# Kernel optimization log

Measured on AMD Instinct MI355X. Metric: run time of the kernel, lower is better.

## Reference

```python
import jax, jax.numpy as jnp
import numpy as np

COMMITMENT_COST = 0.25


def setup_inputs() -> dict:
    key = jax.random.key(0)
    k1, k2 = jax.random.split(key)
    z_e = jax.random.normal(k1, (32, 256, 32, 32), dtype=jnp.float32)
    codebook = jax.random.normal(k2, (1024, 256), dtype=jnp.float32)
    return {"z_e": z_e, "codebook": codebook}


def reference(z_e, codebook):
    B, D, H, W = z_e.shape
    # (B, D, H, W) -> (N, D), N = B*H*W
    z_flat = jnp.transpose(z_e, (0, 2, 3, 1)).reshape(-1, D)
    # squared L2 distances to every codebook entry: (N, K)
    distances = (
        jnp.sum(z_flat * z_flat, axis=1, keepdims=True)
        - 2.0 * (z_flat @ codebook.T)
        + jnp.sum(codebook * codebook, axis=1)
    )
    codes = jnp.argmin(distances, axis=1)          # (N,)
    z_q = jnp.transpose(codebook[codes].reshape(B, H, W, D), (0, 3, 1, 2))
    # straight-through estimator
    z_q_st = z_e + jax.lax.stop_gradient(z_q - z_e)
    codebook_loss = jnp.mean((jax.lax.stop_gradient(z_q) - z_e) ** 2)
    commitment_loss = jnp.mean((z_q - jax.lax.stop_gradient(z_e)) ** 2)
    vq_loss = codebook_loss + COMMITMENT_COST * commitment_loss
    indices = codes.reshape(B, H, W)
    return z_q_st, indices, vq_loss
```

## Files before the change

### kernel.cpp

```cpp
#include <hip/hip_runtime.h>
#include <cstdint>
#include <cstddef>


typedef __attribute__((ext_vector_type(8))) short bf16x8;
typedef __attribute__((ext_vector_type(4))) float f32x4;

#define GL2LDS(g, l) __builtin_amdgcn_global_load_lds( \
    (__attribute__((address_space(1))) const void*)(g), \
    (__attribute__((address_space(3))) void*)(l), 16, 0, 0)

__device__ __forceinline__ unsigned short rne_bf16(float f) {
    unsigned u = __float_as_uint(f);
    return (unsigned short)((u + 0x7FFFu + ((u >> 16) & 1u)) >> 16);
}
__device__ __forceinline__ float bf16_to_f(unsigned short h) {
    return __uint_as_float((unsigned)h << 16);
}

__global__ __launch_bounds__(256)
void vq_cnorm_kernel(const float* __restrict__ cb, float* __restrict__ cnorm)
{
    const int k = blockIdx.x * 256 + threadIdx.x;
    const float4* row = reinterpret_cast<const float4*>(cb + (size_t)k * 256);
    float s0 = 0.f, s1 = 0.f, s2 = 0.f, s3 = 0.f;
#pragma unroll 8
    for (int i = 0; i < 64; ++i) {
        float4 v = row[i];
        s0 = fmaf(v.x, v.x, s0);
        s1 = fmaf(v.y, v.y, s1);
        s2 = fmaf(v.z, v.z, s2);
        s3 = fmaf(v.w, v.w, s3);
    }
    cnorm[k] = (s0 + s1) + (s2 + s3);
}

__global__ __launch_bounds__(256)
void vq_csplit_kernel(const float* __restrict__ cb, unsigned short* __restrict__ c0,
                      unsigned short* __restrict__ c1, unsigned short* __restrict__ c2,
                      unsigned long long* __restrict__ packed, float* __restrict__ loss)
{
    const int b = blockIdx.x, t = threadIdx.x;
    const int idx = b * 256 + t;
    if (t < 128) packed[b * 128 + t] = 0xFFFFFFFFFFFFFFFFull;
    if (b == 0 && t == 255) *loss = 0.f;

    float4 v = reinterpret_cast<const float4*>(cb)[idx];
    float f[4] = { v.x, v.y, v.z, v.w };
    ushort4 h0, h1, h2;
    unsigned short* p0[4] = { &h0.x, &h0.y, &h0.z, &h0.w };
    unsigned short* p1[4] = { &h1.x, &h1.y, &h1.z, &h1.w };
    unsigned short* p2[4] = { &h2.x, &h2.y, &h2.z, &h2.w };
#pragma unroll
    for (int j = 0; j < 4; ++j) {
        unsigned short b0 = rne_bf16(f[j]); float r1 = f[j] - bf16_to_f(b0);
        unsigned short b1 = rne_bf16(r1);   float r2 = r1 - bf16_to_f(b1);
        unsigned short b2 = rne_bf16(r2);
        *p0[j] = b0; *p1[j] = b1; *p2[j] = b2;
    }
    reinterpret_cast<ushort4*>(c0)[idx] = h0;
    reinterpret_cast<ushort4*>(c1)[idx] = h1;
    reinterpret_cast<ushort4*>(c2)[idx] = h2;
}

__global__ __launch_bounds__(256)
void vq_zsplit_kernel(const float* __restrict__ z, unsigned short* __restrict__ z0,
                      unsigned short* __restrict__ z1, unsigned short* __restrict__ z2)
{
    __shared__ float zl[64 * 264];
    const int t = threadIdx.x, blk = blockIdx.x;
    const int b = blk >> 4, hw0 = (blk & 15) << 6;
    const float* zb = z + ((size_t)b << 18) + hw0;
#pragma unroll 8
    for (int i = 0; i < 64; ++i) {
        int idx = i * 256 + t;
        int d = idx >> 6, hwl = idx & 63;
        zl[hwl * 264 + d] = zb[(size_t)d * 1024 + hwl];
    }
    __syncthreads();
    const int n0 = (b << 10) + hw0;
#pragma unroll
    for (int p = 0; p < 8; ++p) {
        const int hwl = p * 8 + (t >> 5);
        const int d0 = (t & 31) * 8;
        const float* src = &zl[hwl * 264 + d0];
        unsigned short h0[8], h1[8], h2[8];
#pragma unroll
        for (int j = 0; j < 8; ++j) {
            float f = src[j];
            unsigned short b0 = rne_bf16(f);  float r1 = f - bf16_to_f(b0);
            unsigned short b1 = rne_bf16(r1); float r2 = r1 - bf16_to_f(b1);
            unsigned short b2 = rne_bf16(r2);
            h0[j] = b0; h1[j] = b1; h2[j] = b2;
        }
        const size_t o = (size_t)(n0 + hwl) * 256 + d0;
        ushort4 a;
        a = ushort4{h0[0],h0[1],h0[2],h0[3]}; *reinterpret_cast<ushort4*>(z0 + o)     = a;
        a = ushort4{h0[4],h0[5],h0[6],h0[7]}; *reinterpret_cast<ushort4*>(z0 + o + 4) = a;
        a = ushort4{h1[0],h1[1],h1[2],h1[3]}; *reinterpret_cast<ushort4*>(z1 + o)     = a;
        a = ushort4{h1[4],h1[5],h1[6],h1[7]}; *reinterpret_cast<ushort4*>(z1 + o + 4) = a;
        a = ushort4{h2[0],h2[1],h2[2],h2[3]}; *reinterpret_cast<ushort4*>(z2 + o)     = a;
        a = ushort4{h2[4],h2[5],h2[6],h2[7]}; *reinterpret_cast<ushort4*>(z2 + o + 4) = a;
    }
}

__global__ __launch_bounds__(512, 1)
void vq_mfma_argmin_kernel(const unsigned short* __restrict__ zp,
                           const unsigned short* __restrict__ cp,
                           const float* __restrict__ cnorm,
                           unsigned long long* __restrict__ packed)
{
    __shared__ unsigned short Ld[3 * 24576];

    const int tid = threadIdx.x, l = tid & 63, w = tid >> 6;
    const int wr = w >> 1, wc = w & 1;
    const int nid = ((blockIdx.x & 7) << 7) | (blockIdx.x >> 3);
    const int bm = nid >> 3, bn = nid & 7;
    const int arow = bm * 256, brow = bn * 128;

    f32x4 acc[4][4];
#pragma unroll
    for (int m = 0; m < 4; ++m)
#pragma unroll
        for (int n = 0; n < 4; ++n) acc[m][n] = f32x4{0.f, 0.f, 0.f, 0.f};

    const int srow  = l >> 2;
    const int selem = (((l & 3) ^ ((l >> 3) & 3))) << 3;

    const int lo16 = l & 15, hi4 = l >> 4;
    const int fco = ((hi4 ^ ((lo16 >> 1) & 3))) << 3;

#define STAGE6(tt, BUFP) do {                                                 \
    const int seg_ = (tt) >> 2;                                               \
    const unsigned short* As_ = zp + (size_t)((0x010210 >> (seg_ << 2)) & 3) * 8388608u; \
    const unsigned short* Bs_ = cp + (size_t)((0x211000 >> (seg_ << 2)) & 3) * 262144u;  \
    const int KO_ = (((tt) & 3) << 6) + selem;                                \
    GL2LDS(As_ + (size_t)(arow + w * 32 +  0 + srow) * 256 + KO_,      (BUFP) + (w * 32     ) * 32); \
    GL2LDS(As_ + (size_t)(arow + w * 32 + 16 + srow) * 256 + KO_,      (BUFP) + (w * 32 + 16) * 32); \
    GL2LDS(As_ + (size_t)(arow + w * 32 +  0 + srow) * 256 + KO_ + 32, (BUFP) + 8192 + (w * 32     ) * 32); \
    GL2LDS(As_ + (size_t)(arow + w * 32 + 16 + srow) * 256 + KO_ + 32, (BUFP) + 8192 + (w * 32 + 16) * 32); \
    GL2LDS(Bs_ + (size_t)(brow + w * 16 + srow) * 256 + KO_,           (BUFP) + 16384 + (w * 16) * 32); \
    GL2LDS(Bs_ + (size_t)(brow + w * 16 + srow) * 256 + KO_ + 32,      (BUFP) + 16384 + 4096 + (w * 16) * 32); \
} while (0)

#define VM6  asm volatile("s_waitcnt vmcnt(6)"  ::: "memory")
#define VM0  asm volatile("s_waitcnt vmcnt(0)"  ::: "memory")
#define NOPS ((void)0)
#define FNCE do { asm volatile("" ::: "memory");                              \
                  __builtin_amdgcn_sched_barrier(0); } while (0)
#define SBAR do { asm volatile("" ::: "memory");                              \
                  __builtin_amdgcn_s_barrier();                               \
                  __builtin_amdgcn_sched_barrier(0); } while (0)

#define MFMA16(A0, A1, A2, A3, B0, B1, B2, B3)                                \
    acc[0][0] = __builtin_amdgcn_mfma_f32_16x16x32_bf16(A0, B0, acc[0][0], 0,0,0); \
    acc[0][1] = __builtin_amdgcn_mfma_f32_16x16x32_bf16(A0, B1, acc[0][1], 0,0,0); \
    acc[0][2] = __builtin_amdgcn_mfma_f32_16x16x32_bf16(A0, B2, acc[0][2], 0,0,0); \
    acc[0][3] = __builtin_amdgcn_mfma_f32_16x16x32_bf16(A0, B3, acc[0][3], 0,0,0); \
    acc[1][0] = __builtin_amdgcn_mfma_f32_16x16x32_bf16(A1, B0, acc[1][0], 0,0,0); \
    acc[1][1] = __builtin_amdgcn_mfma_f32_16x16x32_bf16(A1, B1, acc[1][1], 0,0,0); \
    acc[1][2] = __builtin_amdgcn_mfma_f32_16x16x32_bf16(A1, B2, acc[1][2], 0,0,0); \
    acc[1][3] = __builtin_amdgcn_mfma_f32_16x16x32_bf16(A1, B3, acc[1][3], 0,0,0); \
    acc[2][0] = __builtin_amdgcn_mfma_f32_16x16x32_bf16(A2, B0, acc[2][0], 0,0,0); \
    acc[2][1] = __builtin_amdgcn_mfma_f32_16x16x32_bf16(A2, B1, acc[2][1], 0,0,0); \
    acc[2][2] = __builtin_amdgcn_mfma_f32_16x16x32_bf16(A2, B2, acc[2][2], 0,0,0); \
    acc[2][3] = __builtin_amdgcn_mfma_f32_16x16x32_bf16(A2, B3, acc[2][3], 0,0,0); \
    acc[3][0] = __builtin_amdgcn_mfma_f32_16x16x32_bf16(A3, B0, acc[3][0], 0,0,0); \
    acc[3][1] = __builtin_amdgcn_mfma_f32_16x16x32_bf16(A3, B1, acc[3][1], 0,0,0); \
    acc[3][2] = __builtin_amdgcn_mfma_f32_16x16x32_bf16(A3, B2, acc[3][2], 0,0,0); \
    acc[3][3] = __builtin_amdgcn_mfma_f32_16x16x32_bf16(A3, B3, acc[3][3], 0,0,0)

#define PH_T(BUFP, STAGESTMT, VMSTMT, BARSTMT) do {                           \
    const unsigned short* Ap_ = (BUFP);                                       \
    const unsigned short* Bp_ = (BUFP) + 16384;                               \
    bf16x8 a0, a1, a2, a3, b0, b1, b2, b3;                                    \
    a0 = *(const bf16x8*)&Ap_[(wr*64 + 0*16 + lo16)*32 + fco];                \
    a1 = *(const bf16x8*)&Ap_[(wr*64 + 1*16 + lo16)*32 + fco];                \
    a2 = *(const bf16x8*)&Ap_[(wr*64 + 2*16 + lo16)*32 + fco];                \
    a3 = *(const bf16x8*)&Ap_[(wr*64 + 3*16 + lo16)*32 + fco];                \
    b0 = *(const bf16x8*)&Bp_[(wc*64 + 0*16 + lo16)*32 + fco];                \
    b1 = *(const bf16x8*)&Bp_[(wc*64 + 1*16 + lo16)*32 + fco];                \
    b2 = *(const bf16x8*)&Bp_[(wc*64 + 2*16 + lo16)*32 + fco];                \
    b3 = *(const bf16x8*)&Bp_[(wc*64 + 3*16 + lo16)*32 + fco];                \
    STAGESTMT;                                                                \
    FNCE;                                                                     \
    __builtin_amdgcn_s_setprio(1);                                            \
    MFMA16(a0, a1, a2, a3, b0, b1, b2, b3);                                   \
    __builtin_amdgcn_s_setprio(0);                                            \
    a0 = *(const bf16x8*)&Ap_[8192 + (wr*64 + 0*16 + lo16)*32 + fco];         \
    a1 = *(const bf16x8*)&Ap_[8192 + (wr*64 + 1*16 + lo16)*32 + fco];         \
    a2 = *(const bf16x8*)&Ap_[8192 + (wr*64 + 2*16 + lo16)*32 + fco];         \
    a3 = *(const bf16x8*)&Ap_[8192 + (wr*64 + 3*16 + lo16)*32 + fco];         \
    b0 = *(const bf16x8*)&Bp_[4096 + (wc*64 + 0*16 + lo16)*32 + fco];         \
    b1 = *(const bf16x8*)&Bp_[4096 + (wc*64 + 1*16 + lo16)*32 + fco];         \
    b2 = *(const bf16x8*)&Bp_[4096 + (wc*64 + 2*16 + lo16)*32 + fco];         \
    b3 = *(const bf16x8*)&Bp_[4096 + (wc*64 + 3*16 + lo16)*32 + fco];         \
    FNCE;                                                                     \
    __builtin_amdgcn_s_setprio(1);                                            \
    MFMA16(a0, a1, a2, a3, b0, b1, b2, b3);                                   \
    __builtin_amdgcn_s_setprio(0);                                            \
    VMSTMT;                                                                   \
    BARSTMT;                                                                  \
} while (0)

    STAGE6(0, Ld);
    STAGE6(1, Ld + 24576);
    VM6;
    SBAR;

    for (int t = 0; t < 21; t += 3) {
        PH_T(Ld,             STAGE6(t + 2, Ld + 2 * 24576), VM6, SBAR);
        PH_T(Ld + 24576,     STAGE6(t + 3, Ld),             VM6, SBAR);
        PH_T(Ld + 2 * 24576, STAGE6(t + 4, Ld + 24576),     VM6, SBAR);
    }
    PH_T(Ld,             STAGE6(23, Ld + 2 * 24576), VM6, SBAR);
    PH_T(Ld + 24576,     NOPS,                       VM0, SBAR);
    PH_T(Ld + 2 * 24576, NOPS,                       NOPS, NOPS);

#undef PH_T
#undef MFMA16
#undef STAGE6

    int coln[4]; float cnv[4];
#pragma unroll
    for (int n = 0; n < 4; ++n) {
        coln[n] = brow + wc * 64 + n * 16 + lo16;
        cnv[n] = cnorm[coln[n]];
    }
#pragma unroll
    for (int m = 0; m < 4; ++m) {
#pragma unroll
        for (int j = 0; j < 4; ++j) {
            unsigned long long best = 0xFFFFFFFFFFFFFFFFull;
#pragma unroll
            for (int n = 0; n < 4; ++n) {
                float d = fmaf(-2.0f, acc[m][n][j], cnv[n]);
                unsigned u = __float_as_uint(d);
                u = (u & 0x80000000u) ? ~u : (u | 0x80000000u);
                unsigned long long pk = ((unsigned long long)u << 32) | (unsigned)coln[n];
                best = pk < best ? pk : best;
            }
#pragma unroll
            for (int mask = 1; mask <= 8; mask <<= 1) {
                unsigned long long o = __shfl_xor(best, mask, 64);
                best = o < best ? o : best;
            }
            if (lo16 == 0) {
                const int row = arow + wr * 64 + m * 16 + hi4 * 4 + j;
                atomicMin(&packed[row], best);
            }
        }
    }
}

__global__ __launch_bounds__(256, 2)
void vq_gather_packed_kernel(const float* __restrict__ cb, const float* __restrict__ z,
                             const unsigned long long* __restrict__ packed,
                             float* __restrict__ out_zq, float* __restrict__ out_idx,
                             float* __restrict__ loss)
{
    __shared__ float rows[64 * 257];
    __shared__ int   ks[64];
    __shared__ float wsum[4];

    const int t   = threadIdx.x;
    const int blk = blockIdx.x;
    const int b   = blk >> 4;
    const int hw0 = (blk & 15) << 6;
    const int n0  = blk << 6;

    if (t < 64) {
        const int k = (int)(packed[n0 + t] & 0xFFFFFFFFull);
        ks[t] = k;
        out_idx[n0 + t] = (float)k;
    }
    __syncthreads();

#pragma unroll 4
    for (int i = 0; i < 64; ++i) {
        rows[i * 257 + t] = cb[(size_t)ks[i] * 256 + t];
    }
    __syncthreads();

    const int dq = t >> 6;
    const int hw = t & 63;
    const size_t obase = ((size_t)b << 18) + hw0 + hw;
    float sum = 0.f;
#pragma unroll 4
    for (int dd = 0; dd < 64; ++dd) {
        const int d = (dq << 6) + dd;
        const float  q  = rows[hw * 257 + d];
        const size_t a  = obase + (size_t)d * 1024;
        const float  zv = z[a];
        out_zq[a] = q;
        const float diff = q - zv;
        sum = fmaf(diff, diff, sum);
    }
#pragma unroll
    for (int m = 1; m <= 32; m <<= 1) sum += __shfl_xor(sum, m, 64);
    if ((t & 63) == 0) wsum[t >> 6] = sum;
    __syncthreads();
    if (t == 0) {
        const float s = (wsum[0] + wsum[1]) + (wsum[2] + wsum[3]);
        atomicAdd(loss, s * (1.25f / 8388608.0f));
    }
}

__global__ __launch_bounds__(256)
void vq_transpose_kernel(const float* __restrict__ cb, float* __restrict__ ctT)
{
    __shared__ float tile[64 * 65];
    const int t  = threadIdx.x;
    const int kb = blockIdx.x >> 2, db = blockIdx.x & 3;
    const int k0 = kb << 6, d0 = db << 6;
#pragma unroll
    for (int i = 0; i < 16; ++i) {
        int idx = i * 256 + t;
        int r = idx >> 6, c = idx & 63;
        tile[r * 65 + c] = cb[(size_t)(k0 + r) * 256 + d0 + c];
    }
    __syncthreads();
#pragma unroll
    for (int i = 0; i < 16; ++i) {
        int idx = i * 256 + t;
        int r = idx >> 6, c = idx & 63;
        ctT[(size_t)(d0 + r) * 1024 + k0 + c] = tile[c * 65 + r];
    }
}

__global__ __launch_bounds__(256)
void vq_cnorm_fb_kernel(const float* __restrict__ cb, float* __restrict__ cnorm)
{
    const int k = blockIdx.x * 256 + threadIdx.x;
    const float4* row = reinterpret_cast<const float4*>(cb + (size_t)k * 256);
    float s0 = 0.f, s1 = 0.f, s2 = 0.f, s3 = 0.f;
#pragma unroll 8
    for (int i = 0; i < 64; ++i) {
        float4 v = row[i];
        s0 = fmaf(v.x, v.x, s0);
        s1 = fmaf(v.y, v.y, s1);
        s2 = fmaf(v.z, v.z, s2);
        s3 = fmaf(v.w, v.w, s3);
    }
    cnorm[k] = (s0 + s1) + (s2 + s3);
}

__global__ __launch_bounds__(512, 2)
void vq_argmin_kernel(const float* __restrict__ z, const float* __restrict__ ctT,
                      const float* __restrict__ cnorm, int* __restrict__ codes,
                      float* __restrict__ out_idx)
{
    __shared__ float zt[256 * 64];
    __shared__ float ct[16 * 256];
    const int t = threadIdx.x, tx = t & 63, ty = t >> 6, p0 = ty << 3;
    const int blk = blockIdx.x, b = blk >> 4, hw0 = (blk & 15) << 6;
    const float* zbase = z + ((size_t)b << 18) + hw0;
#pragma unroll
    for (int i = 0; i < 8; ++i) {
        int idx = i * 512 + t;
        int d = idx >> 4, c4 = (idx & 15) << 2;
        float4 v = *reinterpret_cast<const float4*>(zbase + (size_t)d * 1024 + c4);
        *reinterpret_cast<float4*>(&zt[d * 64 + c4]) = v;
    }
    float minv[8]; int mini[8];
#pragma unroll
    for (int i = 0; i < 8; ++i) { minv[i] = 3.0e38f; mini[i] = 0; }
    const float* zrd = &zt[p0];
    const float* crd = &ct[tx << 2];
    for (int kt = 0; kt < 4; ++kt) {
        const int k0 = kt << 8;
        float acc[8][4];
#pragma unroll
        for (int i = 0; i < 8; ++i)
#pragma unroll
            for (int j = 0; j < 4; ++j) acc[i][j] = 0.f;
        for (int dc = 0; dc < 16; ++dc) {
            const int d0 = dc << 4;
            __syncthreads();
#pragma unroll
            for (int i = 0; i < 2; ++i) {
                int idx = i * 512 + t;
                int r = idx >> 6, c4 = (idx & 63) << 2;
                float4 v = *reinterpret_cast<const float4*>(ctT + (size_t)(d0 + r) * 1024 + k0 + c4);
                *reinterpret_cast<float4*>(&ct[r * 256 + c4]) = v;
            }
            __syncthreads();
            const float* zp = zrd + d0 * 64;
#pragma unroll
            for (int d = 0; d < 16; ++d) {
                float4 za = *reinterpret_cast<const float4*>(zp + d * 64);
                float4 zb = *reinterpret_cast<const float4*>(zp + d * 64 + 4);
                float4 cc = *reinterpret_cast<const float4*>(crd + d * 256);
#define VQ_FMA_ROW(ii, zv)                          \
                acc[ii][0] = fmaf(zv, cc.x, acc[ii][0]); \
                acc[ii][1] = fmaf(zv, cc.y, acc[ii][1]); \
                acc[ii][2] = fmaf(zv, cc.z, acc[ii][2]); \
                acc[ii][3] = fmaf(zv, cc.w, acc[ii][3]);
                VQ_FMA_ROW(0, za.x) VQ_FMA_ROW(1, za.y) VQ_FMA_ROW(2, za.z) VQ_FMA_ROW(3, za.w)
                VQ_FMA_ROW(4, zb.x) VQ_FMA_ROW(5, zb.y) VQ_FMA_ROW(6, zb.z) VQ_FMA_ROW(7, zb.w)
#undef VQ_FMA_ROW
            }
        }
#pragma unroll
        for (int j = 0; j < 4; ++j) {
            const int k = k0 + (tx << 2) + j;
            const float cn = cnorm[k];
#pragma unroll
            for (int i = 0; i < 8; ++i) {
                float dist = fmaf(-2.0f, acc[i][j], cn);
                if (dist < minv[i]) { minv[i] = dist; mini[i] = k; }
            }
        }
    }
#pragma unroll
    for (int m = 1; m <= 32; m <<= 1) {
#pragma unroll
        for (int i = 0; i < 8; ++i) {
            float ov = __shfl_xor(minv[i], m, 64);
            int   oi = __shfl_xor(mini[i], m, 64);
            if (ov < minv[i] || (ov == minv[i] && oi < mini[i])) { minv[i] = ov; mini[i] = oi; }
        }
    }
    if (tx == 0) {
        const int n0 = (blk << 6) + p0;
#pragma unroll
        for (int i = 0; i < 8; ++i) {
            codes[n0 + i]   = mini[i];
            out_idx[n0 + i] = (float)mini[i];
        }
    }
}

__global__ __launch_bounds__(256, 2)
void vq_gather_kernel(const float* __restrict__ cb, const float* __restrict__ z,
                      const int* __restrict__ codes, float* __restrict__ out_zq,
                      float* __restrict__ loss)
{
    __shared__ float rows[64 * 257];
    __shared__ int   ks[64];
    __shared__ float wsum[4];
    const int t = threadIdx.x, blk = blockIdx.x;
    const int b = blk >> 4, hw0 = (blk & 15) << 6, n0 = blk << 6;
    if (t < 64) ks[t] = codes[n0 + t];
    __syncthreads();
#pragma unroll 4
    for (int i = 0; i < 64; ++i) rows[i * 257 + t] = cb[(size_t)ks[i] * 256 + t];
    __syncthreads();
    const int dq = t >> 6, hw = t & 63;
    const size_t obase = ((size_t)b << 18) + hw0 + hw;
    float sum = 0.f;
#pragma unroll 4
    for (int dd = 0; dd < 64; ++dd) {
        const int d = (dq << 6) + dd;
        const float  q  = rows[hw * 257 + d];
        const size_t a  = obase + (size_t)d * 1024;
        const float  zv = z[a];
        out_zq[a] = q;
        const float diff = q - zv;
        sum = fmaf(diff, diff, sum);
    }
#pragma unroll
    for (int m = 1; m <= 32; m <<= 1) sum += __shfl_xor(sum, m, 64);
    if ((t & 63) == 0) wsum[t >> 6] = sum;
    __syncthreads();
    if (t == 0) {
        const float s = (wsum[0] + wsum[1]) + (wsum[2] + wsum[3]);
        atomicAdd(loss, s * (1.25f / 8388608.0f));
    }
}

extern "C" void kernel_launch(void* const* d_in, const int* in_sizes, int n_in,
                              void* d_out, int out_size, void* d_ws, size_t ws_size,
                              hipStream_t stream)
{
    (void)in_sizes; (void)n_in; (void)out_size;

    const float* z  = (const float*)d_in[0];
    const float* cb = (const float*)d_in[1];

    float* out      = (float*)d_out;
    float* out_zq   = out;
    float* out_idx  = out + 8388608;
    float* out_loss = out + 8421376;

    const size_t NEED = 262144ull + 3ull * 16777216ull + 3ull * 524288ull + 4096ull;

    if (ws_size >= NEED) {
        unsigned long long* packed = (unsigned long long*)d_ws;
        unsigned short* z0 = (unsigned short*)((char*)d_ws + 262144);
        unsigned short* z1 = z0 + 8388608u;
        unsigned short* z2 = z1 + 8388608u;
        unsigned short* c0 = z2 + 8388608u;
        unsigned short* c1 = c0 + 262144u;
        unsigned short* c2 = c1 + 262144u;
        float* cnorm = (float*)(c2 + 262144u);

        vq_csplit_kernel<<<256, 256, 0, stream>>>(cb, c0, c1, c2, packed, out_loss);
        vq_cnorm_kernel<<<4, 256, 0, stream>>>(cb, cnorm);
        vq_zsplit_kernel<<<512, 256, 0, stream>>>(z, z0, z1, z2);
        vq_mfma_argmin_kernel<<<1024, 512, 0, stream>>>(z0, c0, cnorm, packed);
        vq_gather_packed_kernel<<<512, 256, 0, stream>>>(cb, z, packed, out_zq, out_idx, out_loss);
    } else {
        float* ctT   = (float*)d_ws;
        float* cnorm = ctT + 256 * 1024;
        int*   codes = (int*)(cnorm + 1024);

        hipMemsetAsync(out_loss, 0, sizeof(float), stream);
        vq_transpose_kernel<<<64, 256, 0, stream>>>(cb, ctT);
        vq_cnorm_fb_kernel<<<4, 256, 0, stream>>>(cb, cnorm);
        vq_argmin_kernel<<<512, 512, 0, stream>>>(z, ctT, cnorm, codes, out_idx);
        vq_gather_kernel<<<512, 256, 0, stream>>>(cb, z, codes, out_zq, out_loss);
    }
}
```

Before: 180.1 us.

## Software-pipeline LDS fragment reads with double-buffered registers across MFMA halves

Restructures the main GEMM loop so the LDS reads for the next half-tile (and the next buffer's first half) are issued before the current MFMA block runs, using two register sets (x/y). This is meant to hide LDS read latency behind MFMA execution instead of stalling on each read group. It removes the explicit sched_barrier fences, adds an lgkmcnt(0) wait before the barrier, and raises register pressure from the extra 16 bf16x8 fragment registers.

```diff
diff --git a/kernel.cpp b/kernel.cpp
--- a/kernel.cpp
+++ b/kernel.cpp
@@ -145,12 +145,25 @@
 
 #define VM6  asm volatile("s_waitcnt vmcnt(6)"  ::: "memory")
 #define VM0  asm volatile("s_waitcnt vmcnt(0)"  ::: "memory")
+#define LK0  asm volatile("s_waitcnt lgkmcnt(0)" ::: "memory")
 #define NOPS ((void)0)
-#define FNCE do { asm volatile("" ::: "memory");                              \
-                  __builtin_amdgcn_sched_barrier(0); } while (0)
 #define SBAR do { asm volatile("" ::: "memory");                              \
                   __builtin_amdgcn_s_barrier();                               \
                   __builtin_amdgcn_sched_barrier(0); } while (0)
+
+    bf16x8 xa0, xa1, xa2, xa3, xb0, xb1, xb2, xb3;
+    bf16x8 ya0, ya1, ya2, ya3, yb0, yb1, yb2, yb3;
+
+#define READ_A(d0, d1, d2, d3, PLANE)                                         \
+    d0 = *(const bf16x8*)&(PLANE)[(wr*64 + 0*16 + lo16)*32 + fco];            \
+    d1 = *(const bf16x8*)&(PLANE)[(wr*64 + 1*16 + lo16)*32 + fco];            \
+    d2 = *(const bf16x8*)&(PLANE)[(wr*64 + 2*16 + lo16)*32 + fco];            \
+    d3 = *(const bf16x8*)&(PLANE)[(wr*64 + 3*16 + lo16)*32 + fco]
+#define READ_B(d0, d1, d2, d3, PLANE)                                         \
+    d0 = *(const bf16x8*)&(PLANE)[(wc*64 + 0*16 + lo16)*32 + fco];            \
+    d1 = *(const bf16x8*)&(PLANE)[(wc*64 + 1*16 + lo16)*32 + fco];            \
+    d2 = *(const bf16x8*)&(PLANE)[(wc*64 + 2*16 + lo16)*32 + fco];            \
+    d3 = *(const bf16x8*)&(PLANE)[(wc*64 + 3*16 + lo16)*32 + fco]
 
 #define MFMA16(A0, A1, A2, A3, B0, B1, B2, B3)                                \
     acc[0][0] = __builtin_amdgcn_mfma_f32_16x16x32_bf16(A0, B0, acc[0][0], 0,0,0); \
@@ -170,55 +183,47 @@
     acc[3][2] = __builtin_amdgcn_mfma_f32_16x16x32_bf16(A3, B2, acc[3][2], 0,0,0); \
     acc[3][3] = __builtin_amdgcn_mfma_f32_16x16x32_bf16(A3, B3, acc[3][3], 0,0,0)
 
-#define PH_T(BUFP, STAGESTMT, VMSTMT, BARSTMT) do {                           \
-    const unsigned short* Ap_ = (BUFP);                                       \
-    const unsigned short* Bp_ = (BUFP) + 16384;                               \
-    bf16x8 a0, a1, a2, a3, b0, b1, b2, b3;                                    \
-    a0 = *(const bf16x8*)&Ap_[(wr*64 + 0*16 + lo16)*32 + fco];                \
-    a1 = *(const bf16x8*)&Ap_[(wr*64 + 1*16 + lo16)*32 + fco];                \
-    a2 = *(const bf16x8*)&Ap_[(wr*64 + 2*16 + lo16)*32 + fco];                \
-    a3 = *(const bf16x8*)&Ap_[(wr*64 + 3*16 + lo16)*32 + fco];                \
-    b0 = *(const bf16x8*)&Bp_[(wc*64 + 0*16 + lo16)*32 + fco];                \
-    b1 = *(const bf16x8*)&Bp_[(wc*64 + 1*16 + lo16)*32 + fco];                \
-    b2 = *(const bf16x8*)&Bp_[(wc*64 + 2*16 + lo16)*32 + fco];                \
-    b3 = *(const bf16x8*)&Bp_[(wc*64 + 3*16 + lo16)*32 + fco];                \
+#define PH(BUFC, BUFN, STAGESTMT, VMSTMT, BARSTMT, RDNEXT) do {               \
+         \
+    READ_A(ya0, ya1, ya2, ya3, (BUFC) + 8192);                                \
+    READ_B(yb0, yb1, yb2, yb3, (BUFC) + 16384 + 4096);                        \
     STAGESTMT;                                                                \
-    FNCE;                                                                     \
     __builtin_amdgcn_s_setprio(1);                                            \
-    MFMA16(a0, a1, a2, a3, b0, b1, b2, b3);                                   \
+    MFMA16(xa0, xa1, xa2, xa3, xb0, xb1, xb2, xb3);                           \
     __builtin_amdgcn_s_setprio(0);                                            \
-    a0 = *(const bf16x8*)&Ap_[8192 + (wr*64 + 0*16 + lo16)*32 + fco];         \
-    a1 = *(const bf16x8*)&Ap_[8192 + (wr*64 + 1*16 + lo16)*32 + fco];         \
-    a2 = *(const bf16x8*)&Ap_[8192 + (wr*64 + 2*16 + lo16)*32 + fco];         \
-    a3 = *(const bf16x8*)&Ap_[8192 + (wr*64 + 3*16 + lo16)*32 + fco];         \
-    b0 = *(const bf16x8*)&Bp_[4096 + (wc*64 + 0*16 + lo16)*32 + fco];         \
-    b1 = *(const bf16x8*)&Bp_[4096 + (wc*64 + 1*16 + lo16)*32 + fco];         \
-    b2 = *(const bf16x8*)&Bp_[4096 + (wc*64 + 2*16 + lo16)*32 + fco];         \
-    b3 = *(const bf16x8*)&Bp_[4096 + (wc*64 + 3*16 + lo16)*32 + fco];         \
-    FNCE;                                                                     \
-    __builtin_amdgcn_s_setprio(1);                                            \
-    MFMA16(a0, a1, a2, a3, b0, b1, b2, b3);                                   \
-    __builtin_amdgcn_s_setprio(0);                                            \
+    LK0;                                                                      \
     VMSTMT;                                                                   \
     BARSTMT;                                                                  \
+          \
+    if (RDNEXT) {                                                             \
+        READ_A(xa0, xa1, xa2, xa3, (BUFN));                                   \
+        READ_B(xb0, xb1, xb2, xb3, (BUFN) + 16384);                           \
+    }                                                                         \
+    __builtin_amdgcn_s_setprio(1);                                            \
+    MFMA16(ya0, ya1, ya2, ya3, yb0, yb1, yb2, yb3);                           \
+    __builtin_amdgcn_s_setprio(0);                                            \
 } while (0)
 
     STAGE6(0, Ld);
     STAGE6(1, Ld + 24576);
     VM6;
     SBAR;
+    READ_A(xa0, xa1, xa2, xa3, Ld);
+    READ_B(xb0, xb1, xb2, xb3, Ld + 16384);
 
     for (int t = 0; t < 21; t += 3) {
-        PH_T(Ld,             STAGE6(t + 2, Ld + 2 * 24576), VM6, SBAR);
-        PH_T(Ld + 24576,     STAGE6(t + 3, Ld),             VM6, SBAR);
-        PH_T(Ld + 2 * 24576, STAGE6(t + 4, Ld + 24576),     VM6, SBAR);
-    }
-    PH_T(Ld,             STAGE6(23, Ld + 2 * 24576), VM6, SBAR);
-    PH_T(Ld + 24576,     NOPS,                       VM0, SBAR);
-    PH_T(Ld + 2 * 24576, NOPS,                       NOPS, NOPS);
-
-#undef PH_T
+        PH(Ld,             Ld + 24576,     STAGE6(t + 2, Ld + 2 * 24576), VM6, SBAR, 1);
+        PH(Ld + 24576,     Ld + 2 * 24576, STAGE6(t + 3, Ld),             VM6, SBAR, 1);
+        PH(Ld + 2 * 24576, Ld,             STAGE6(t + 4, Ld + 24576),     VM6, SBAR, 1);
+    }
+    PH(Ld,             Ld + 24576,     STAGE6(23, Ld + 2 * 24576), VM6, SBAR, 1);
+    PH(Ld + 24576,     Ld + 2 * 24576, NOPS,                       VM0, SBAR, 1);
+    PH(Ld + 2 * 24576, Ld,             NOPS,                       NOPS, NOPS, 0);
+
+#undef PH
 #undef MFMA16
+#undef READ_A
+#undef READ_B
 #undef STAGE6
 
     int coln[4]; float cnv[4];
```

Result: faster. 172.6 us (-4.2%).
